# Kernel optimization log

Hardware: AMD Instinct MI355X
Metric: run time of the kernel (lower is better)

Reference implementation:

```python
import jax, jax.numpy as jnp
import numpy as np

B, T, C = 4, 2048, 1024
H, D = 16, 64


def setup_inputs() -> dict:
    key = jax.random.key(0)
    ks = jax.random.split(key, 5)
    x = jax.random.normal(ks[0], (B, T, C), dtype=jnp.float32)
    Wq = jax.random.normal(ks[1], (H, C, D), dtype=jnp.float32) * (C ** -0.5)
    Wk = jax.random.normal(ks[2], (H, C, D), dtype=jnp.float32) * (C ** -0.5)
    Wv = jax.random.normal(ks[3], (H, C, D), dtype=jnp.float32) * (C ** -0.5)
    Wp = jax.random.normal(ks[4], (H * D, C), dtype=jnp.float32) * ((H * D) ** -0.5)
    bp = jnp.zeros((C,), dtype=jnp.float32)
    return {"x": x, "Wq": Wq, "Wk": Wk, "Wv": Wv, "Wp": Wp, "bp": bp}


def reference(x, Wq, Wk, Wv, Wp, bp):
    # per-head projections (bias-free): [B,H,T,D]
    q = jnp.einsum('btc,hcd->bhtd', x, Wq)
    k = jnp.einsum('btc,hcd->bhtd', x, Wk)
    v = jnp.einsum('btc,hcd->bhtd', x, Wv)
    # NOTE: source multiplies by sqrt(head_size) (faithful to original code)
    scale = jnp.asarray(D ** 0.5, x.dtype)
    att = jnp.einsum('bhtd,bhsd->bhts', q, k) * scale  # [B,H,T,T]
    causal = jnp.tril(jnp.ones((T, T), dtype=bool))
    att = jnp.where(causal, att, jnp.asarray(-jnp.inf, att.dtype))
    att = jax.nn.softmax(att, axis=-1)
    out = jnp.einsum('bhts,bhsd->bhtd', att, v)  # [B,H,T,D]
    out = out.transpose(0, 2, 1, 3).reshape(B, T, H * D)  # head concat
    return out @ Wp + bp
```

## Files before the change

### kernel.cpp

```cpp
#include <hip/hip_runtime.h>

#define B_ 4
#define T_ 2048
#define C_ 1024
#define H_ 16
#define D_ 64

typedef _Float16 f16x8 __attribute__((ext_vector_type(8)));
typedef __fp16 fp16x2 __attribute__((ext_vector_type(2)));
typedef float f32x4 __attribute__((ext_vector_type(4)));
typedef unsigned short u16x8 __attribute__((ext_vector_type(8)));

#define MFMA16 __builtin_amdgcn_mfma_f32_16x16x32_f16
#define SCALE2 11.541560327111707f

__device__ __forceinline__ unsigned pk2(float a, float b) {
    fp16x2 p = __builtin_amdgcn_cvt_pkrtz(a, b);
    return __builtin_bit_cast(unsigned, p);
}

__device__ __forceinline__ void gl_lds16(const _Float16* g, unsigned short* lds) {
    __builtin_amdgcn_global_load_lds(
        (const __attribute__((address_space(1))) unsigned int*)g,
        (__attribute__((address_space(3))) unsigned int*)lds, 16, 0, 0);
}

__global__ __launch_bounds__(256) void convx_kernel(const float* __restrict__ x,
                                                    _Float16* __restrict__ Xf) {
    size_t i = ((size_t)blockIdx.x * 256 + threadIdx.x) * 8;
    f32x4 a = *reinterpret_cast<const f32x4*>(x + i);
    f32x4 b = *reinterpret_cast<const f32x4*>(x + i + 4);
    f16x8 o;
    o[0] = (_Float16)a[0]; o[1] = (_Float16)a[1]; o[2] = (_Float16)a[2]; o[3] = (_Float16)a[3];
    o[4] = (_Float16)b[0]; o[5] = (_Float16)b[1]; o[6] = (_Float16)b[2]; o[7] = (_Float16)b[3];
    *reinterpret_cast<f16x8*>(Xf + i) = o;
}

__global__ __launch_bounds__(256) void convw_qkv_kernel(
    const float* __restrict__ Wq, const float* __restrict__ Wk, const float* __restrict__ Wv,
    _Float16* __restrict__ Wqt, _Float16* __restrict__ Wkt, _Float16* __restrict__ Wvt)
{
    __shared__ unsigned short Wl[128][72];
    const int ct = blockIdx.x, h = blockIdx.y, m = blockIdx.z;
    const float* src = (m == 0 ? Wq : (m == 1 ? Wk : Wv)) + ((size_t)h * C_ + ct * 128) * D_;
    _Float16* dst = (m == 0 ? Wqt : (m == 1 ? Wkt : Wvt));
    const int tid = threadIdx.x;
    {
        int r = tid >> 1, half = tid & 1;
        #pragma unroll
        for (int i = 0; i < 8; i++) {
            f32x4 v = *reinterpret_cast<const f32x4*>(src + (size_t)r * D_ + half * 32 + i * 4);
            #pragma unroll
            for (int j = 0; j < 4; j++)
                Wl[r][half * 32 + i * 4 + j] = __builtin_bit_cast(unsigned short, (_Float16)v[j]);
        }
    }
    __syncthreads();
    {
        int d = tid >> 2, seg = tid & 3;
        #pragma unroll
        for (int i = 0; i < 4; i++) {
            u16x8 o;
            #pragma unroll
            for (int j = 0; j < 8; j++) o[j] = Wl[seg * 32 + i * 8 + j][d];
            *reinterpret_cast<u16x8*>((unsigned short*)dst + ((size_t)h * D_ + d) * C_ + ct * 128 + seg * 32 + i * 8) = o;
        }
    }
}

__global__ __launch_bounds__(256) void convw_p_kernel(const float* __restrict__ Wp,
                                                      _Float16* __restrict__ Wpt)
{
    __shared__ unsigned short Pl[64][72];
    const int jt = blockIdx.x, kt = blockIdx.y;
    const int tid = threadIdx.x;
    {
        int r = tid >> 2, seg = tid & 3;
        #pragma unroll
        for (int i = 0; i < 4; i++) {
            f32x4 v = *reinterpret_cast<const f32x4*>(Wp + (size_t)(kt * 64 + r) * C_ + jt * 64 + seg * 16 + i * 4);
            #pragma unroll
            for (int j = 0; j < 4; j++)
                Pl[r][seg * 16 + i * 4 + j] = __builtin_bit_cast(unsigned short, (_Float16)v[j]);
        }
    }
    __syncthreads();
    {
        int jj = tid >> 2, kseg = tid & 3;
        #pragma unroll
        for (int i = 0; i < 2; i++) {
            u16x8 o;
            #pragma unroll
            for (int j = 0; j < 8; j++) o[j] = Pl[kseg * 16 + i * 8 + j][jj];
            *reinterpret_cast<u16x8*>((unsigned short*)Wpt + (size_t)(jt * 64 + jj) * C_ + kt * 64 + kseg * 16 + i * 8) = o;
        }
    }
}

__global__ __launch_bounds__(256) void qkv2_kernel(
    const _Float16* __restrict__ Xf, const _Float16* __restrict__ Wcat,
    _Float16* __restrict__ Qf, _Float16* __restrict__ Kf, _Float16* __restrict__ Vt)
{
    __shared__ unsigned short As[128 * 64];
    __shared__ unsigned short Bs[128 * 64];
    const int rt = blockIdx.x, ct = blockIdx.y;
    const int row0 = rt * 128, n0 = ct * 128;
    const int tid = threadIdx.x, wid = tid >> 6, lane = tid & 63;
    const int l15 = lane & 15, g = lane >> 4;
    const int wr = wid >> 1, wc = wid & 1;
    const int lrow = lane >> 3, lcol = (lane & 7) * 8;

    f32x4 acc[4][4];
    #pragma unroll
    for (int mi = 0; mi < 4; mi++)
        #pragma unroll
        for (int ni = 0; ni < 4; ni++) { f32x4 z = {0.f,0.f,0.f,0.f}; acc[mi][ni] = z; }

    for (int k0 = 0; k0 < C_; k0 += 64) {
        __syncthreads();
        #pragma unroll
        for (int i = 0; i < 4; i++) {
            int c = wid * 4 + i;
            gl_lds16(Xf   + (size_t)(row0 + c * 8 + lrow) * C_ + k0 + lcol, &As[c * 512]);
            gl_lds16(Wcat + (size_t)(n0   + c * 8 + lrow) * C_ + k0 + lcol, &Bs[c * 512]);
        }
        __syncthreads();
        #pragma unroll
        for (int kk = 0; kk < 2; kk++) {
            f16x8 af[4], bf[4];
            #pragma unroll
            for (int mi = 0; mi < 4; mi++)
                af[mi] = *reinterpret_cast<const f16x8*>(&As[(wr * 64 + mi * 16 + l15) * 64 + kk * 32 + g * 8]);
            #pragma unroll
            for (int ni = 0; ni < 4; ni++)
                bf[ni] = *reinterpret_cast<const f16x8*>(&Bs[(wc * 64 + ni * 16 + l15) * 64 + kk * 32 + g * 8]);
            #pragma unroll
            for (int mi = 0; mi < 4; mi++)
                #pragma unroll
                for (int ni = 0; ni < 4; ni++)
                    acc[mi][ni] = MFMA16(af[mi], bf[ni], acc[mi][ni], 0, 0, 0);
        }
    }

    const int n0w = n0 + wc * 64;
    const int h = (n0w >> 6) & 15;
    const int b = row0 >> 11;
    const int t0b = (row0 & (T_ - 1)) + wr * 64;

    if (ct < 16) {
        _Float16* dst = (ct < 8) ? Qf : Kf;
        const float osc = (ct < 8) ? SCALE2 : 1.0f;
        const size_t hb = ((size_t)(b * H_ + h)) * T_ * D_;
        #pragma unroll
        for (int mi = 0; mi < 4; mi++)
            #pragma unroll
            for (int ni = 0; ni < 4; ni++) {
                int d = ni * 16 + l15;
                #pragma unroll
                for (int r = 0; r < 4; r++) {
                    int t = t0b + mi * 16 + g * 4 + r;
                    dst[hb + (size_t)t * D_ + d] = (_Float16)(acc[mi][ni][r] * osc);
                }
            }
    } else {
        const size_t vbase = ((size_t)(b * H_ + h)) * D_ * T_;
        #pragma unroll
        for (int mi = 0; mi < 4; mi++)
            #pragma unroll
            for (int ni = 0; ni < 4; ni++) {
                int d = ni * 16 + l15;
                int t = t0b + mi * 16 + g * 4;
                uint2 w;
                w.x = pk2(acc[mi][ni][0], acc[mi][ni][1]);
                w.y = pk2(acc[mi][ni][2], acc[mi][ni][3]);
                *reinterpret_cast<uint2*>((unsigned short*)Vt + vbase + (size_t)d * T_ + t) = w;
            }
    }
}

__global__ __launch_bounds__(256) void flash_kernel(
    const _Float16* __restrict__ Qf, const _Float16* __restrict__ Kf,
    const _Float16* __restrict__ Vt, _Float16* __restrict__ att)
{
    __shared__ __align__(16) unsigned short Ks[2][64 * 64];
    __shared__ __align__(16) unsigned short Vs[2][64 * 64];
    __shared__ __align__(16) unsigned short Ps[4][32 * 32];
    const int bh = blockIdx.x;
    const int qt = 15 - (int)blockIdx.y;
    const int bb = bh >> 4, h = bh & 15;
    const int tid = threadIdx.x, wid = tid >> 6, lane = tid & 63;
    const int l15 = lane & 15, g = lane >> 4;
    const int q0 = qt * 128;
    const int qw = q0 + wid * 32;

    const _Float16* Qb = Qf + (size_t)bh * T_ * D_;
    const _Float16* Kb = Kf + (size_t)bh * T_ * D_;
    const _Float16* Vb = Vt + (size_t)bh * D_ * T_;

    const int srow = lane >> 3;
    const int sunit = (lane & 7) ^ srow;
    const int r0s = wid * 16;

    f16x8 qf[2][2];
    #pragma unroll
    for (int mt = 0; mt < 2; mt++)
        #pragma unroll
        for (int kk = 0; kk < 2; kk++)
            qf[mt][kk] = *reinterpret_cast<const f16x8*>(Qb + (size_t)(qw + mt * 16 + l15) * D_ + kk * 32 + g * 8);

    f32x4 accO[4][2];
    #pragma unroll
    for (int nt = 0; nt < 4; nt++)
        #pragma unroll
        for (int mt = 0; mt < 2; mt++) { f32x4 z = {0.f,0.f,0.f,0.f}; accO[nt][mt] = z; }
    float m[2] = { -1e30f, -1e30f };
    float l[2] = { 0.f, 0.f };

    const int myNt = (qw + 95) >> 6;
    const int ntB  = (q0 + 191) >> 6;

    #pragma unroll
    for (int i = 0; i < 2; i++) {
        int row = r0s + i * 8 + srow;
        gl_lds16(Kb + (size_t)row * D_ + sunit * 8, &Ks[0][(r0s + i * 8) * 64]);
        gl_lds16(Vb + (size_t)row * T_ + sunit * 8, &Vs[0][(r0s + i * 8) * 64]);
    }
    __syncthreads();

    char* const pbase = (char*)&Ps[wid][0];

#define TILE_BODY(TI, BUF)                                                          \
    {                                                                               \
        const int kv0 = (TI) * 64;                                                  \
        if ((TI) + 1 < ntB) {                                                       \
            const int kvn = kv0 + 64;                                               \
            _Pragma("unroll")                                                       \
            for (int i = 0; i < 2; i++) {                                           \
                int row = r0s + i * 8 + srow;                                       \
                gl_lds16(Kb + (size_t)(kvn + row) * D_ + sunit * 8,                 \
                         &Ks[(BUF) ^ 1][(r0s + i * 8) * 64]);                       \
                gl_lds16(Vb + (size_t)row * T_ + kvn + sunit * 8,                   \
                         &Vs[(BUF) ^ 1][(r0s + i * 8) * 64]);                       \
            }                                                                       \
        }                                                                           \
        if ((TI) < myNt) {                                                          \
            const bool maskt = ((TI) == myNt - 1);                                  \
            const char* kbase = (const char*)&Ks[BUF][0];                           \
            const char* vbase = (const char*)&Vs[BUF][0];                           \
            f32x4 s[4][2];                                                          \
            _Pragma("unroll")                                                       \
            for (int st = 0; st < 4; st++)                                          \
                _Pragma("unroll")                                                   \
                for (int mt = 0; mt < 2; mt++) { f32x4 z = {0.f,0.f,0.f,0.f}; s[st][mt] = z; } \
            _Pragma("unroll")                                                       \
            for (int kk = 0; kk < 2; kk++) {                                        \
                f16x8 kfr[4];                                                       \
                _Pragma("unroll")                                                   \
                for (int st = 0; st < 4; st++) {                                    \
                    int row = st * 16 + l15;                                        \
                    kfr[st] = *reinterpret_cast<const f16x8*>(                      \
                        kbase + row * 128 + (((kk * 4 + g) ^ (row & 7)) * 16));     \
                }                                                                   \
                _Pragma("unroll")                                                   \
                for (int st = 0; st < 4; st++)                                      \
                    _Pragma("unroll")                                               \
                    for (int mt = 0; mt < 2; mt++)                                  \
                        s[st][mt] = MFMA16(kfr[st], qf[mt][kk], s[st][mt], 0, 0, 0);\
            }                                                                       \
            unsigned pw[2][4][2];                                                   \
            _Pragma("unroll")                                                       \
            for (int mt = 0; mt < 2; mt++) {                                        \
                const int r = mt * 16 + l15;                                        \
                const int qrow = qw + r;                                            \
                float lv[4][4];                                                     \
                float vmax = -1e30f;                                                \
                _Pragma("unroll")                                                   \
                for (int st = 0; st < 4; st++)                                      \
                    _Pragma("unroll")                                               \
                    for (int rr = 0; rr < 4; rr++) {                                \
                        float v = s[st][mt][rr];                                    \
                        if (maskt) {                                                \
                            int kv = kv0 + st * 16 + g * 4 + rr;                    \
                            v = (kv <= qrow) ? v : -1e30f;                          \
                        }                                                           \
                        lv[st][rr] = v;                                             \
                        vmax = fmaxf(vmax, v);                                      \
                    }                                                               \
                vmax = fmaxf(vmax, __shfl_xor(vmax, 16, 64));                       \
                vmax = fmaxf(vmax, __shfl_xor(vmax, 32, 64));                       \
                float mnew = fmaxf(m[mt], vmax);                                    \
                float alpha = __builtin_amdgcn_exp2f(m[mt] - mnew);                 \
                m[mt] = mnew;                                                       \
                float rs = 0.f;                                                     \
                _Pragma("unroll")                                                   \
                for (int st = 0; st < 4; st++) {                                    \
                    float p0 = __builtin_amdgcn_exp2f(lv[st][0] - mnew);            \
                    float p1 = __builtin_amdgcn_exp2f(lv[st][1] - mnew);            \
                    float p2 = __builtin_amdgcn_exp2f(lv[st][2] - mnew);            \
                    float p3 = __builtin_amdgcn_exp2f(lv[st][3] - mnew);            \
                    rs += (p0 + p1) + (p2 + p3);                                    \
                    pw[mt][st][0] = pk2(p0, p1);                                    \
                    pw[mt][st][1] = pk2(p2, p3);                                    \
                }                                                                   \
                rs += __shfl_xor(rs, 16, 64);                                       \
                rs += __shfl_xor(rs, 32, 64);                                       \
                l[mt] = l[mt] * alpha + rs;                                         \
                _Pragma("unroll")                                                   \
                for (int nt = 0; nt < 4; nt++) accO[nt][mt] *= alpha;               \
            }                                                                       \
            _Pragma("unroll")                                                       \
            for (int half = 0; half < 2; half++) {                                  \
                _Pragma("unroll")                                                   \
                for (int mt = 0; mt < 2; mt++) {                                    \
                    const int r = mt * 16 + l15;                                    \
                    const int swz = ((r >> 1) & 3) << 4;                            \
                    char* prow = pbase + r * 64;                                    \
                    _Pragma("unroll")                                               \
                    for (int stl = 0; stl < 2; stl++) {                             \
                        uint2 w;                                                    \
                        w.x = pw[mt][half * 2 + stl][0];                            \
                        w.y = pw[mt][half * 2 + stl][1];                            \
                        *reinterpret_cast<uint2*>(prow + ((stl * 32 + g * 8) ^ swz)) = w; \
                    }                                                               \
                }                                                                   \
                f16x8 pb[2];                                                        \
                _Pragma("unroll")                                                   \
                for (int mt = 0; mt < 2; mt++) {                                    \
                    const int r = mt * 16 + l15;                                    \
                    const int swz = ((r >> 1) & 3) << 4;                            \
                    pb[mt] = *reinterpret_cast<const f16x8*>(pbase + r * 64 + ((g * 16) ^ swz)); \
                }                                                                   \
                _Pragma("unroll")                                                   \
                for (int nt = 0; nt < 4; nt++) {                                    \
                    int row = nt * 16 + l15;                                        \
                    f16x8 vf = *reinterpret_cast<const f16x8*>(                     \
                        vbase + row * 128 + (((half * 4 + g) ^ (row & 7)) * 16));   \
                    _Pragma("unroll")                                               \
                    for (int mt = 0; mt < 2; mt++)                                  \
                        accO[nt][mt] = MFMA16(vf, pb[mt], accO[nt][mt], 0, 0, 0);   \
                }                                                                   \
            }                                                                       \
        }                                                                           \
        __syncthreads();                                                            \
    }

    for (int tI = 0; tI < ntB; tI += 2) {
        TILE_BODY(tI, 0)
        if (tI + 1 < ntB) {
            TILE_BODY(tI + 1, 1)
        }
    }
#undef TILE_BODY

    #pragma unroll
    for (int mt = 0; mt < 2; mt++) {
        float inv = 1.0f / l[mt];
        int t = qw + mt * 16 + l15;
        #pragma unroll
        for (int nt = 0; nt < 4; nt++) {
            f32x4 o = accO[nt][mt] * inv;
            uint2 w;
            w.x = pk2(o[0], o[1]);
            w.y = pk2(o[2], o[3]);
            size_t off = ((size_t)(bb * T_ + t)) * (H_ * D_) + h * D_ + nt * 16 + g * 4;
            *reinterpret_cast<uint2*>((unsigned short*)att + off) = w;
        }
    }
}

__global__ __launch_bounds__(256) void proj2_kernel(
    const _Float16* __restrict__ att, const _Float16* __restrict__ Wpt,
    const float* __restrict__ bp, float* __restrict__ out)
{
    __shared__ unsigned short As[128 * 64];
    __shared__ unsigned short Bs[128 * 64];
    const int rt = blockIdx.x, ct = blockIdx.y;
    const int row0 = rt * 128, n0 = ct * 128;
    const int tid = threadIdx.x, wid = tid >> 6, lane = tid & 63;
    const int l15 = lane & 15, g = lane >> 4;
    const int wr = wid >> 1, wc = wid & 1;
    const int lrow = lane >> 3, lcol = (lane & 7) * 8;

    f32x4 acc[4][4];
    #pragma unroll
    for (int mi = 0; mi < 4; mi++)
        #pragma unroll
        for (int ni = 0; ni < 4; ni++) { f32x4 z = {0.f,0.f,0.f,0.f}; acc[mi][ni] = z; }

    for (int k0 = 0; k0 < C_; k0 += 64) {
        __syncthreads();
        #pragma unroll
        for (int i = 0; i < 4; i++) {
            int c = wid * 4 + i;
            gl_lds16(att + (size_t)(row0 + c * 8 + lrow) * C_ + k0 + lcol, &As[c * 512]);
            gl_lds16(Wpt + (size_t)(n0   + c * 8 + lrow) * C_ + k0 + lcol, &Bs[c * 512]);
        }
        __syncthreads();
        #pragma unroll
        for (int kk = 0; kk < 2; kk++) {
            f16x8 af[4], bf[4];
            #pragma unroll
            for (int mi = 0; mi < 4; mi++)
                af[mi] = *reinterpret_cast<const f16x8*>(&As[(wr * 64 + mi * 16 + l15) * 64 + kk * 32 + g * 8]);
            #pragma unroll
            for (int ni = 0; ni < 4; ni++)
                bf[ni] = *reinterpret_cast<const f16x8*>(&Bs[(wc * 64 + ni * 16 + l15) * 64 + kk * 32 + g * 8]);
            #pragma unroll
            for (int mi = 0; mi < 4; mi++)
                #pragma unroll
                for (int ni = 0; ni < 4; ni++)
                    acc[mi][ni] = MFMA16(af[mi], bf[ni], acc[mi][ni], 0, 0, 0);
        }
    }

    #pragma unroll
    for (int mi = 0; mi < 4; mi++)
        #pragma unroll
        for (int ni = 0; ni < 4; ni++) {
            int col = n0 + wc * 64 + ni * 16 + l15;
            float bias = bp[col];
            #pragma unroll
            for (int r = 0; r < 4; r++) {
                int row = row0 + wr * 64 + mi * 16 + g * 4 + r;
                out[(size_t)row * C_ + col] = acc[mi][ni][r] + bias;
            }
        }
}

extern "C" void kernel_launch(void* const* d_in, const int* in_sizes, int n_in,
                              void* d_out, int out_size, void* d_ws, size_t ws_size,
                              hipStream_t stream) {
    const float* x  = (const float*)d_in[0];
    const float* Wq = (const float*)d_in[1];
    const float* Wk = (const float*)d_in[2];
    const float* Wv = (const float*)d_in[3];
    const float* Wp = (const float*)d_in[4];
    const float* bp = (const float*)d_in[5];
    float* out = (float*)d_out;

    _Float16* Xf  = (_Float16*)d_ws;
    _Float16* Wqt = Xf  + (size_t)8388608;
    _Float16* Wkt = Wqt + (size_t)1048576;
    _Float16* Wvt = Wkt + (size_t)1048576;
    _Float16* Wpt = Wvt + (size_t)1048576;
    _Float16* Qf  = Wpt + (size_t)1048576;
    _Float16* Kf  = Qf  + (size_t)8388608;
    _Float16* Vt  = Kf  + (size_t)8388608;
    _Float16* att = Vt  + (size_t)8388608;

    convx_kernel<<<4096, 256, 0, stream>>>(x, Xf);
    convw_qkv_kernel<<<dim3(8, 16, 3), 256, 0, stream>>>(Wq, Wk, Wv, Wqt, Wkt, Wvt);
    convw_p_kernel<<<dim3(16, 16), 256, 0, stream>>>(Wp, Wpt);
    qkv2_kernel<<<dim3(64, 24), 256, 0, stream>>>(Xf, Wqt, Qf, Kf, Vt);
    flash_kernel<<<dim3(64, 16), 256, 0, stream>>>(Qf, Kf, Vt, att);
    proj2_kernel<<<dim3(64, 8), 256, 0, stream>>>(att, Wpt, bp, out);
}
```

Baseline: 205.9 us.

## Retile QKV GEMM to 96-wide columns and pair causal query tiles per flash block

The QKV projection GEMM now uses 128x96 output tiles, giving a 64x32 grid of 2048 blocks instead of 1536. This is meant to fill the CUs more evenly across waves, at the cost of a lower MFMA-to-load ratio per block. The flash kernel now processes two query tiles per block, pairing tile 15-p with tile p so each block does roughly equal causal work. This halves the grid to 512 blocks to balance load and cut tail effects, but lowers parallelism, and each block reloads K/V for its second pass.

Measured after the change: 217.1 us. 5.4% more time.

```diff
diff --git a/kernel.cpp b/kernel.cpp
--- a/kernel.cpp
+++ b/kernel.cpp
@@ -97,84 +97,86 @@
     }
 }
 
-__global__ __launch_bounds__(256) void qkv2_kernel(
+__global__ __launch_bounds__(256) void qkv3_kernel(
     const _Float16* __restrict__ Xf, const _Float16* __restrict__ Wcat,
     _Float16* __restrict__ Qf, _Float16* __restrict__ Kf, _Float16* __restrict__ Vt)
 {
     __shared__ unsigned short As[128 * 64];
-    __shared__ unsigned short Bs[128 * 64];
+    __shared__ unsigned short Bs[96 * 64];
     const int rt = blockIdx.x, ct = blockIdx.y;
-    const int row0 = rt * 128, n0 = ct * 128;
+    const int row0 = rt * 128, n0 = ct * 96;
     const int tid = threadIdx.x, wid = tid >> 6, lane = tid & 63;
     const int l15 = lane & 15, g = lane >> 4;
     const int wr = wid >> 1, wc = wid & 1;
     const int lrow = lane >> 3, lcol = (lane & 7) * 8;
 
-    f32x4 acc[4][4];
+    f32x4 acc[4][3];
     #pragma unroll
     for (int mi = 0; mi < 4; mi++)
         #pragma unroll
-        for (int ni = 0; ni < 4; ni++) { f32x4 z = {0.f,0.f,0.f,0.f}; acc[mi][ni] = z; }
+        for (int ni = 0; ni < 3; ni++) { f32x4 z = {0.f,0.f,0.f,0.f}; acc[mi][ni] = z; }
 
     for (int k0 = 0; k0 < C_; k0 += 64) {
         __syncthreads();
         #pragma unroll
         for (int i = 0; i < 4; i++) {
             int c = wid * 4 + i;
-            gl_lds16(Xf   + (size_t)(row0 + c * 8 + lrow) * C_ + k0 + lcol, &As[c * 512]);
-            gl_lds16(Wcat + (size_t)(n0   + c * 8 + lrow) * C_ + k0 + lcol, &Bs[c * 512]);
+            gl_lds16(Xf + (size_t)(row0 + c * 8 + lrow) * C_ + k0 + lcol, &As[c * 512]);
+        }
+        #pragma unroll
+        for (int i = 0; i < 3; i++) {
+            int c = wid * 3 + i;
+            gl_lds16(Wcat + (size_t)(n0 + c * 8 + lrow) * C_ + k0 + lcol, &Bs[c * 512]);
         }
         __syncthreads();
         #pragma unroll
         for (int kk = 0; kk < 2; kk++) {
-            f16x8 af[4], bf[4];
+            f16x8 af[4], bf[3];
             #pragma unroll
             for (int mi = 0; mi < 4; mi++)
                 af[mi] = *reinterpret_cast<const f16x8*>(&As[(wr * 64 + mi * 16 + l15) * 64 + kk * 32 + g * 8]);
             #pragma unroll
-            for (int ni = 0; ni < 4; ni++)
-                bf[ni] = *reinterpret_cast<const f16x8*>(&Bs[(wc * 64 + ni * 16 + l15) * 64 + kk * 32 + g * 8]);
+            for (int ni = 0; ni < 3; ni++)
+                bf[ni] = *reinterpret_cast<const f16x8*>(&Bs[(wc * 48 + ni * 16 + l15) * 64 + kk * 32 + g * 8]);
             #pragma unroll
             for (int mi = 0; mi < 4; mi++)
                 #pragma unroll
-                for (int ni = 0; ni < 4; ni++)
+                for (int ni = 0; ni < 3; ni++)
                     acc[mi][ni] = MFMA16(af[mi], bf[ni], acc[mi][ni], 0, 0, 0);
         }
     }
 
-    const int n0w = n0 + wc * 64;
-    const int h = (n0w >> 6) & 15;
     const int b = row0 >> 11;
     const int t0b = (row0 & (T_ - 1)) + wr * 64;
-
-    if (ct < 16) {
-        _Float16* dst = (ct < 8) ? Qf : Kf;
-        const float osc = (ct < 8) ? SCALE2 : 1.0f;
-        const size_t hb = ((size_t)(b * H_ + h)) * T_ * D_;
-        #pragma unroll
-        for (int mi = 0; mi < 4; mi++)
-            #pragma unroll
-            for (int ni = 0; ni < 4; ni++) {
-                int d = ni * 16 + l15;
+    #pragma unroll
+    for (int ni = 0; ni < 3; ni++) {
+        const int n = n0 + wc * 48 + ni * 16;
+        const int region = n >> 10;
+        const int h = (n >> 6) & 15;
+        const int d0 = n & 63;
+        if (region < 2) {
+            _Float16* dst = region ? Kf : Qf;
+            const float osc = region ? 1.0f : SCALE2;
+            const size_t hb = ((size_t)(b * H_ + h)) * T_ * D_;
+            #pragma unroll
+            for (int mi = 0; mi < 4; mi++)
                 #pragma unroll
                 for (int r = 0; r < 4; r++) {
                     int t = t0b + mi * 16 + g * 4 + r;
-                    dst[hb + (size_t)t * D_ + d] = (_Float16)(acc[mi][ni][r] * osc);
+                    dst[hb + (size_t)t * D_ + d0 + l15] = (_Float16)(acc[mi][ni][r] * osc);
                 }
-            }
-    } else {
-        const size_t vbase = ((size_t)(b * H_ + h)) * D_ * T_;
-        #pragma unroll
-        for (int mi = 0; mi < 4; mi++)
-            #pragma unroll
-            for (int ni = 0; ni < 4; ni++) {
-                int d = ni * 16 + l15;
+        } else {
+            const size_t vbase = ((size_t)(b * H_ + h)) * D_ * T_;
+            const int d = d0 + l15;
+            #pragma unroll
+            for (int mi = 0; mi < 4; mi++) {
                 int t = t0b + mi * 16 + g * 4;
                 uint2 w;
                 w.x = pk2(acc[mi][ni][0], acc[mi][ni][1]);
                 w.y = pk2(acc[mi][ni][2], acc[mi][ni][3]);
                 *reinterpret_cast<uint2*>((unsigned short*)Vt + vbase + (size_t)d * T_ + t) = w;
             }
+        }
     }
 }
 
@@ -186,12 +188,10 @@
     __shared__ __align__(16) unsigned short Vs[2][64 * 64];
     __shared__ __align__(16) unsigned short Ps[4][32 * 32];
     const int bh = blockIdx.x;
-    const int qt = 15 - (int)blockIdx.y;
+    const int p = (int)blockIdx.y;
     const int bb = bh >> 4, h = bh & 15;
     const int tid = threadIdx.x, wid = tid >> 6, lane = tid & 63;
     const int l15 = lane & 15, g = lane >> 4;
-    const int q0 = qt * 128;
-    const int qw = q0 + wid * 32;
 
     const _Float16* Qb = Qf + (size_t)bh * T_ * D_;
     const _Float16* Kb = Kf + (size_t)bh * T_ * D_;
@@ -201,33 +201,38 @@
     const int sunit = (lane & 7) ^ srow;
     const int r0s = wid * 16;
 
-    f16x8 qf[2][2];
-    #pragma unroll
-    for (int mt = 0; mt < 2; mt++)
-        #pragma unroll
-        for (int kk = 0; kk < 2; kk++)
-            qf[mt][kk] = *reinterpret_cast<const f16x8*>(Qb + (size_t)(qw + mt * 16 + l15) * D_ + kk * 32 + g * 8);
-
-    f32x4 accO[4][2];
-    #pragma unroll
-    for (int nt = 0; nt < 4; nt++)
-        #pragma unroll
-        for (int mt = 0; mt < 2; mt++) { f32x4 z = {0.f,0.f,0.f,0.f}; accO[nt][mt] = z; }
-    float m[2] = { -1e30f, -1e30f };
-    float l[2] = { 0.f, 0.f };
-
-    const int myNt = (qw + 95) >> 6;
-    const int ntB  = (q0 + 191) >> 6;
-
-    #pragma unroll
-    for (int i = 0; i < 2; i++) {
-        int row = r0s + i * 8 + srow;
-        gl_lds16(Kb + (size_t)row * D_ + sunit * 8, &Ks[0][(r0s + i * 8) * 64]);
-        gl_lds16(Vb + (size_t)row * T_ + sunit * 8, &Vs[0][(r0s + i * 8) * 64]);
-    }
-    __syncthreads();
-
     char* const pbase = (char*)&Ps[wid][0];
+
+    for (int pass = 0; pass < 2; pass++) {
+        const int qt = pass ? p : (15 - p);
+        const int q0 = qt * 128;
+        const int qw = q0 + wid * 32;
+
+        f16x8 qf[2][2];
+        #pragma unroll
+        for (int mt = 0; mt < 2; mt++)
+            #pragma unroll
+            for (int kk = 0; kk < 2; kk++)
+                qf[mt][kk] = *reinterpret_cast<const f16x8*>(Qb + (size_t)(qw + mt * 16 + l15) * D_ + kk * 32 + g * 8);
+
+        f32x4 accO[4][2];
+        #pragma unroll
+        for (int nt = 0; nt < 4; nt++)
+            #pragma unroll
+            for (int mt = 0; mt < 2; mt++) { f32x4 z = {0.f,0.f,0.f,0.f}; accO[nt][mt] = z; }
+        float m[2] = { -1e30f, -1e30f };
+        float l[2] = { 0.f, 0.f };
+
+        const int myNt = (qw + 95) >> 6;
+        const int ntB  = (q0 + 191) >> 6;
+
+        #pragma unroll
+        for (int i = 0; i < 2; i++) {
+            int row = r0s + i * 8 + srow;
+            gl_lds16(Kb + (size_t)row * D_ + sunit * 8, &Ks[0][(r0s + i * 8) * 64]);
+            gl_lds16(Vb + (size_t)row * T_ + sunit * 8, &Vs[0][(r0s + i * 8) * 64]);
+        }
+        __syncthreads();
 
 #define TILE_BODY(TI, BUF)                                                          \
     {                                                                               \
@@ -344,26 +349,27 @@
         __syncthreads();                                                            \
     }
 
-    for (int tI = 0; tI < ntB; tI += 2) {
-        TILE_BODY(tI, 0)
-        if (tI + 1 < ntB) {
-            TILE_BODY(tI + 1, 1)
-        }
-    }
+        for (int tI = 0; tI < ntB; tI += 2) {
+            TILE_BODY(tI, 0)
+            if (tI + 1 < ntB) {
+                TILE_BODY(tI + 1, 1)
+            }
+        }
 #undef TILE_BODY
 
-    #pragma unroll
-    for (int mt = 0; mt < 2; mt++) {
-        float inv = 1.0f / l[mt];
-        int t = qw + mt * 16 + l15;
-        #pragma unroll
-        for (int nt = 0; nt < 4; nt++) {
-            f32x4 o = accO[nt][mt] * inv;
-            uint2 w;
-            w.x = pk2(o[0], o[1]);
-            w.y = pk2(o[2], o[3]);
-            size_t off = ((size_t)(bb * T_ + t)) * (H_ * D_) + h * D_ + nt * 16 + g * 4;
-            *reinterpret_cast<uint2*>((unsigned short*)att + off) = w;
+        #pragma unroll
+        for (int mt = 0; mt < 2; mt++) {
+            float inv = 1.0f / l[mt];
+            int t = qw + mt * 16 + l15;
+            #pragma unroll
+            for (int nt = 0; nt < 4; nt++) {
+                f32x4 o = accO[nt][mt] * inv;
+                uint2 w;
+                w.x = pk2(o[0], o[1]);
+                w.y = pk2(o[2], o[3]);
+                size_t off = ((size_t)(bb * T_ + t)) * (H_ * D_) + h * D_ + nt * 16 + g * 4;
+                *reinterpret_cast<uint2*>((unsigned short*)att + off) = w;
+            }
         }
     }
 }
@@ -451,7 +457,7 @@
     convx_kernel<<<4096, 256, 0, stream>>>(x, Xf);
     convw_qkv_kernel<<<dim3(8, 16, 3), 256, 0, stream>>>(Wq, Wk, Wv, Wqt, Wkt, Wvt);
     convw_p_kernel<<<dim3(16, 16), 256, 0, stream>>>(Wp, Wpt);
-    qkv2_kernel<<<dim3(64, 24), 256, 0, stream>>>(Xf, Wqt, Qf, Kf, Vt);
-    flash_kernel<<<dim3(64, 16), 256, 0, stream>>>(Qf, Kf, Vt, att);
+    qkv3_kernel<<<dim3(64, 32), 256, 0, stream>>>(Xf, Wqt, Qf, Kf, Vt);
+    flash_kernel<<<dim3(64, 8), 256, 0, stream>>>(Qf, Kf, Vt, att);
     proj2_kernel<<<dim3(64, 8), 256, 0, stream>>>(att, Wpt, bp, out);
 }
```
